# Optimization experiments

Measured on AMD Instinct MI355X. Metric: run time of the kernel, lower is better.

The kernel has to match this reference:

```python
import jax, jax.numpy as jnp
import numpy as np

N_NODES = 20000
N_EDGES = 200000
D_MODEL = 128
N_HEADS = 8
N_LAYERS = 2  # num_gnn - 1 concat layers


def setup_inputs() -> dict:
    key = jax.random.key(0)
    ks = jax.random.split(key, 12)
    s = 0.05  # keep activations well-scaled across residual layers
    hd = D_MODEL // N_HEADS  # 16
    return {
        "x": jax.random.normal(ks[0], (N_NODES, D_MODEL), jnp.float32),
        "src": jax.random.randint(ks[1], (N_EDGES,), 0, N_NODES),
        "dst": jax.random.randint(ks[2], (N_EDGES,), 0, N_NODES),
        "Ws": jax.random.normal(ks[3], (N_LAYERS, D_MODEL, D_MODEL), jnp.float32) * s,
        "als": jax.random.normal(ks[4], (N_LAYERS, N_HEADS, hd), jnp.float32) * s,
        "ars": jax.random.normal(ks[5], (N_LAYERS, N_HEADS, hd), jnp.float32) * s,
        "bs": jax.random.normal(ks[6], (N_LAYERS, D_MODEL), jnp.float32) * s,
        "W_last": jax.random.normal(ks[7], (D_MODEL, N_HEADS * D_MODEL), jnp.float32) * s,
        "al_last": jax.random.normal(ks[8], (N_HEADS, D_MODEL), jnp.float32) * s,
        "ar_last": jax.random.normal(ks[9], (N_HEADS, D_MODEL), jnp.float32) * s,
        "b_last": jax.random.normal(ks[10], (N_HEADS * D_MODEL,), jnp.float32) * s,
    }


def gat_conv(h, src, dst, W, al, ar, b, num_nodes):
    """DGL GATConv (eval mode, dropout off): returns (N, H, D) head outputs."""
    H, D = al.shape
    feat = (h @ W).reshape(num_nodes, H, D)          # (N,H,D)
    el = jnp.sum(feat * al[None], axis=-1)           # (N,H) attn on src side
    er = jnp.sum(feat * ar[None], axis=-1)           # (N,H) attn on dst side
    e = jax.nn.leaky_relu(el[src] + er[dst], 0.2)    # (E,H)
    # edge softmax over incoming edges of each dst node, per head
    m = jax.ops.segment_max(e, dst, num_segments=num_nodes)  # (N,H)
    p = jnp.exp(e - m[dst])                          # (E,H)
    z = jax.ops.segment_sum(p, dst, num_segments=num_nodes)  # (N,H)
    a = p / z[dst]                                   # (E,H)
    msg = feat[src] * a[..., None]                   # (E,H,D) weighted messages
    rst = jax.ops.segment_sum(msg, dst, num_segments=num_nodes)  # (N,H,D)
    return rst + b.reshape(1, H, D)


def reference(x, src, dst, Ws, als, ars, bs, W_last, al_last, ar_last, b_last):
    N = x.shape[0]
    h = x
    for i in range(N_LAYERS):
        temp = gat_conv(h, src, dst, Ws[i], als[i], ars[i], bs[i], N)  # (N,H,hd)
        h = h + jax.nn.elu(temp.reshape(N, -1))       # concat heads, ELU, residual
    temp = gat_conv(h, src, dst, W_last, al_last, ar_last, b_last, N)  # (N,H,D)
    h = h + jnp.mean(temp, axis=1)                    # mean over heads, residual
    return h
```

## Files before the change

kernel.cpp:

```cpp
#include <hip/hip_runtime.h>
#include <math.h>

#define N_NODES 20000
#define N_EDGES 200000
#define DM 128
#define NH 8

typedef __attribute__((ext_vector_type(8))) short bf16x8;
typedef __attribute__((ext_vector_type(4))) float f32x4;

__device__ __forceinline__ unsigned short f2b(float f) {
  unsigned int u = __float_as_uint(f);
  unsigned int r = (u + 0x7FFFu + ((u >> 16) & 1u)) >> 16;
  return (unsigned short)r;
}
__device__ __forceinline__ float b2f(unsigned short s) {
  return __uint_as_float(((unsigned int)s) << 16);
}

__global__ __launch_bounds__(256) void degzero(int* __restrict__ deg) {
  int i = blockIdx.x * 256 + threadIdx.x;
  if (i < N_NODES) deg[i] = 0;
}

__global__ __launch_bounds__(256) void prep_all(
    const float* __restrict__ x, float* __restrict__ h, unsigned short* __restrict__ hb,
    const int* __restrict__ dstE, int* __restrict__ deg, int* __restrict__ rank,
    const float* __restrict__ Ws, unsigned short* __restrict__ wsz,
    const float* __restrict__ W_last, unsigned short* __restrict__ wpsz,
    const float* __restrict__ al_last, const float* __restrict__ ar_last,
    const float* __restrict__ b_last, unsigned short* __restrict__ wlrsz,
    float* __restrict__ mb) {
  int i = blockIdx.x * 256 + threadIdx.x;
  if (i < (N_NODES * DM) / 4) {
    float4 v = ((const float4*)x)[i];
    ((float4*)h)[i] = v;
    ((ushort4*)hb)[i] = make_ushort4(f2b(v.x), f2b(v.y), f2b(v.z), f2b(v.w));
  }
  if (i < N_EDGES) rank[i] = atomicAdd(&deg[dstE[i]], 1);
  if (i < 2 * 16384) {
    int layer = i >> 14;
    int r = i & 16383;
    int j = r & 7, l = (r >> 3) & 63, f = (r >> 9) & 7, ks = r >> 12;
    int k = ks * 32 + ((l >> 4) << 3) + j;
    int n = f * 16 + (l & 15);
    wsz[i] = f2b(Ws[(size_t)layer * 16384 + k * 128 + n]);
  }
  if (i < 131072) {
    int j = i & 7, l = (i >> 3) & 63, f = (i >> 9) & 7, ks = i >> 12;
    int k = ks * 32 + ((l >> 4) << 3) + j;
    int n = f * 16 + (l & 15);
    int h_ = k >> 7, ko = k & 127;
    wpsz[i] = f2b(W_last[(size_t)ko * 1024 + h_ * 128 + n] * 0.125f);
  }
  if (i < 2048) {
    int j = i & 7, l = (i >> 3) & 63, ks = i >> 9;
    int k = ks * 32 + ((l >> 4) << 3) + j;
    int n = l & 15;
    int hh = n & 7;
    const float* av = (n < 8) ? (al_last + hh * 128) : (ar_last + hh * 128);
    float s = 0.f;
    for (int d = 0; d < 128; ++d) s += W_last[(size_t)k * 1024 + hh * 128 + d] * av[d];
    wlrsz[i] = f2b(s);
  }
  if (i < 128) {
    float s = 0.f;
#pragma unroll
    for (int hh = 0; hh < 8; ++hh) s += b_last[hh * 128 + i];
    mb[i] = s * 0.125f;
  }
}

__global__ void scan_deg(const int* __restrict__ deg, int* __restrict__ off) {
  __shared__ int part[1024];
  const int tid = threadIdx.x;
  const int CHUNK = (N_NODES + 1023) / 1024;
  int base = tid * CHUNK;
  int s = 0;
  for (int i = 0; i < CHUNK; ++i) {
    int idx = base + i;
    if (idx < N_NODES) s += deg[idx];
  }
  part[tid] = s;
  __syncthreads();
  for (int ofs = 1; ofs < 1024; ofs <<= 1) {
    int v = (tid >= ofs) ? part[tid - ofs] : 0;
    __syncthreads();
    part[tid] += v;
    __syncthreads();
  }
  int run = (tid > 0) ? part[tid - 1] : 0;
  for (int i = 0; i < CHUNK; ++i) {
    int idx = base + i;
    if (idx < N_NODES) {
      off[idx] = run;
      run += deg[idx];
    }
  }
  if (tid == 0) off[N_NODES] = part[1023];
}

template <int K>
__device__ __forceinline__ void dev_gemm(int tile, const unsigned short* __restrict__ A,
                                         const unsigned short* __restrict__ Bsz,
                                         unsigned short* __restrict__ Cb,
                                         const float* __restrict__ al,
                                         const float* __restrict__ ar,
                                         float* __restrict__ elr, int lane, int wid) {
  const int wrow = wid & 1, wc = wid >> 1;
  const int r0 = tile * 32;
  const int arow = r0 + wrow * 16 + (lane & 15);
  const int kg = lane >> 4;

  f32x4 acc[4];
#pragma unroll
  for (int fi = 0; fi < 4; ++fi) acc[fi] = {0.f, 0.f, 0.f, 0.f};

  const bf16x8* Ap = (const bf16x8*)(A + (size_t)arow * K + kg * 8);
#pragma unroll 4
  for (int ks = 0; ks < K / 32; ++ks) {
    bf16x8 a = Ap[ks * 4];
#pragma unroll
    for (int fi = 0; fi < 4; ++fi) {
      int f = wc * 4 + fi;
      bf16x8 b = *(const bf16x8*)(Bsz + (((size_t)(ks * 8 + f) * 64 + lane) << 3));
      acc[fi] = __builtin_amdgcn_mfma_f32_16x16x32_bf16(a, b, acc[fi], 0, 0, 0);
    }
  }

  const int rbase = r0 + wrow * 16 + (lane >> 4) * 4;
#pragma unroll
  for (int fi = 0; fi < 4; ++fi) {
    int col = wc * 64 + fi * 16 + (lane & 15);
#pragma unroll
    for (int r = 0; r < 4; ++r) {
      Cb[(size_t)(rbase + r) * DM + col] = f2b(acc[fi][r]);
    }
  }

#pragma unroll
  for (int fi = 0; fi < 4; ++fi) {
    int hh = wc * 4 + fi;
    float alv = al[hh * 16 + (lane & 15)];
    float arv = ar[hh * 16 + (lane & 15)];
#pragma unroll
    for (int r = 0; r < 4; ++r) {
      float pl = acc[fi][r] * alv;
      float pr = acc[fi][r] * arv;
#pragma unroll
      for (int msk = 1; msk < 16; msk <<= 1) {
        pl += __shfl_xor(pl, msk, 64);
        pr += __shfl_xor(pr, msk, 64);
      }
      if ((lane & 15) == 0) {
        int row = rbase + r;
        elr[row * 16 + hh] = pl;
        elr[row * 16 + 8 + hh] = pr;
      }
    }
  }
}

__global__ __launch_bounds__(256) void gemm0_scatter(
    const unsigned short* __restrict__ A, const unsigned short* __restrict__ Bsz,
    unsigned short* __restrict__ Cb, const float* __restrict__ al,
    const float* __restrict__ ar, float* __restrict__ elr, const int* __restrict__ srcE,
    const int* __restrict__ dstE, const int* __restrict__ rank,
    const int* __restrict__ off, int* __restrict__ csr_src) {
  const int bid = blockIdx.x;
  if (bid < N_NODES / 32) {
    dev_gemm<DM>(bid, A, Bsz, Cb, al, ar, elr, threadIdx.x & 63, threadIdx.x >> 6);
  } else {
    int e = (bid - N_NODES / 32) * 256 + threadIdx.x;
    if (e < N_EDGES) {
      csr_src[off[dstE[e]] + rank[e]] = srcE[e];
    }
  }
}

__global__ __launch_bounds__(256) void gemm_mfma(
    const unsigned short* __restrict__ A, const unsigned short* __restrict__ Bsz,
    unsigned short* __restrict__ Cb, const float* __restrict__ al,
    const float* __restrict__ ar, float* __restrict__ elr) {
  dev_gemm<DM>(blockIdx.x, A, Bsz, Cb, al, ar, elr, threadIdx.x & 63, threadIdx.x >> 6);
}

template <bool ELR>
__global__ __launch_bounds__(256) void fused_small(
    const int* __restrict__ off, const int* __restrict__ csr_src,
    const unsigned short* __restrict__ feat, const float* __restrict__ elr,
    const float* __restrict__ bias, float* __restrict__ h, unsigned short* __restrict__ hb,
    const unsigned short* __restrict__ wlrsz, float* __restrict__ elr_out) {
  __shared__ float a_lds[4][64];
  __shared__ int s_lds[4][8];
  __shared__ float zi_lds[4][8];
  __shared__ __align__(16) unsigned short nh_lds[4][128];
  const int wid = threadIdx.x >> 6;
  const int t = blockIdx.x * 4 + wid;
  const int lane = threadIdx.x & 63;
  const int e_loc = lane >> 3, hh = lane & 7;
  const int hg = lane >> 3;
  const int beg = off[t], end = off[t + 1];
  const float ert = elr[t * 16 + 8 + hh];

  int e = beg + e_loc;
  bool val = e < end;
  int s = val ? csr_src[e] : 0;
  float xl = val ? elr[s * 16 + hh] : 0.f;

  float z = 0.f, acc0 = 0.f, acc1 = 0.f;
  for (int base = beg; base < end; base += 8) {
    float ex = 0.f;
    if (val) {
      float xv = xl + ert;
      xv = xv > 0.f ? xv : 0.2f * xv;
      ex = __expf(xv);
    }
    a_lds[wid][lane] = ex;
    if (hh == 0) s_lds[wid][e_loc] = s;
    __builtin_amdgcn_wave_barrier();
    asm volatile("s_waitcnt lgkmcnt(0)" ::: "memory");
    z += ex;
    int en = base + 8 + e_loc;
    bool valn = en < end;
    int sn = valn ? csr_src[en] : 0;
    float xln = valn ? elr[sn * 16 + hh] : 0.f;
    int n = min(8, end - base);
    for (int e2 = 0; e2 < n; ++e2) {
      int s2 = s_lds[wid][e2];
      float a = a_lds[wid][e2 * 8 + hg];
      unsigned int hv = *(const unsigned int*)&feat[(size_t)s2 * 128 + 2 * lane];
      acc0 += a * b2f((unsigned short)(hv & 0xffffu));
      acc1 += a * b2f((unsigned short)(hv >> 16));
    }
    __builtin_amdgcn_wave_barrier();
    s = sn;
    xl = xln;
    val = valn;
  }
  z += __shfl_xor(z, 8, 64);
  z += __shfl_xor(z, 16, 64);
  z += __shfl_xor(z, 32, 64);
  if (e_loc == 0) zi_lds[wid][hh] = (z > 0.f) ? 1.f / z : 0.f;
  __builtin_amdgcn_wave_barrier();
  asm volatile("s_waitcnt lgkmcnt(0)" ::: "memory");
  float zi = zi_lds[wid][hg];

  float2 bv = *(const float2*)&bias[2 * lane];
  float v0 = acc0 * zi + bv.x;
  float v1 = acc1 * zi + bv.y;
  v0 = v0 > 0.f ? v0 : expm1f(v0);
  v1 = v1 > 0.f ? v1 : expm1f(v1);
  size_t idx = (size_t)t * 128 + 2 * lane;
  float2 hv = *(const float2*)&h[idx];
  float nh0 = hv.x + v0;
  float nh1 = hv.y + v1;
  *(float2*)&h[idx] = make_float2(nh0, nh1);
  unsigned short b0 = f2b(nh0), b1 = f2b(nh1);
  *(ushort2*)&hb[idx] = make_ushort2(b0, b1);

  if (ELR) {
    *(ushort2*)&nh_lds[wid][2 * lane] = make_ushort2(b0, b1);
    __builtin_amdgcn_wave_barrier();
    asm volatile("s_waitcnt lgkmcnt(0)" ::: "memory");
    const int kg = lane >> 4;
    f32x4 acc = {0.f, 0.f, 0.f, 0.f};
#pragma unroll
    for (int ks = 0; ks < 4; ++ks) {
      bf16x8 a = *(const bf16x8*)&nh_lds[wid][ks * 32 + kg * 8];
      bf16x8 b = *(const bf16x8*)(wlrsz + (((size_t)ks * 64 + lane) << 3));
      acc = __builtin_amdgcn_mfma_f32_16x16x32_bf16(a, b, acc, 0, 0, 0);
    }
    if (lane < 16) elr_out[t * 16 + lane] = acc[0];
  }
}

#define GT_STRIDE 1032
__global__ __launch_bounds__(1024) void agg_gemm16(
    const int* __restrict__ off, const int* __restrict__ csr_src,
    const unsigned short* __restrict__ hb, const float* __restrict__ elr,
    const unsigned short* __restrict__ wpsz, const float* __restrict__ hres,
    const float* __restrict__ mb, float* __restrict__ out) {
  __shared__ __align__(16) unsigned short gt[16][GT_STRIDE];
  __shared__ float red[8][64][4];
  __shared__ float a_lds[16][64];
  __shared__ int s_lds[16][8];
  __shared__ float zi_lds[16][8];
  const int wid = threadIdx.x >> 6;
  const int lane = threadIdx.x & 63;
  const int t0 = blockIdx.x * 16;
  const int t = t0 + wid;
  const int e_loc = lane >> 3, hh = lane & 7;

  {
    const int beg = off[t], end = off[t + 1];
    const float ert = elr[t * 16 + 8 + hh];
    int e = beg + e_loc;
    bool val = e < end;
    int s = val ? csr_src[e] : 0;
    float xl = val ? elr[s * 16 + hh] : 0.f;

    float z = 0.f;
    float accA[8], accB[8];
#pragma unroll
    for (int k = 0; k < 8; ++k) accA[k] = accB[k] = 0.f;

    for (int base = beg; base < end; base += 8) {
      float ex = 0.f;
      if (val) {
        float xv = xl + ert;
        xv = xv > 0.f ? xv : 0.2f * xv;
        ex = __expf(xv);
      }
      a_lds[wid][lane] = ex;
      if (hh == 0) s_lds[wid][e_loc] = s;
      __builtin_amdgcn_wave_barrier();
      asm volatile("s_waitcnt lgkmcnt(0)" ::: "memory");
      z += ex;
      int en = base + 8 + e_loc;
      bool valn = en < end;
      int sn = valn ? csr_src[en] : 0;
      float xln = valn ? elr[sn * 16 + hh] : 0.f;
      int n = min(8, end - base);
      for (int e2 = 0; e2 < n; ++e2) {
        int s2 = s_lds[wid][e2];
        float4 pa = *(const float4*)&a_lds[wid][e2 * 8];
        float4 pb = *(const float4*)&a_lds[wid][e2 * 8 + 4];
        unsigned int hv = *(const unsigned int*)&hb[(size_t)s2 * 128 + 2 * lane];
        float h0 = b2f((unsigned short)(hv & 0xffffu));
        float h1 = b2f((unsigned short)(hv >> 16));
        accA[0] += pa.x * h0; accB[0] += pa.x * h1;
        accA[1] += pa.y * h0; accB[1] += pa.y * h1;
        accA[2] += pa.z * h0; accB[2] += pa.z * h1;
        accA[3] += pa.w * h0; accB[3] += pa.w * h1;
        accA[4] += pb.x * h0; accB[4] += pb.x * h1;
        accA[5] += pb.y * h0; accB[5] += pb.y * h1;
        accA[6] += pb.z * h0; accB[6] += pb.z * h1;
        accA[7] += pb.w * h0; accB[7] += pb.w * h1;
      }
      __builtin_amdgcn_wave_barrier();
      s = sn;
      xl = xln;
      val = valn;
    }
    z += __shfl_xor(z, 8, 64);
    z += __shfl_xor(z, 16, 64);
    z += __shfl_xor(z, 32, 64);
    if (e_loc == 0) zi_lds[wid][hh] = (z > 0.f) ? 1.f / z : 0.f;
    __builtin_amdgcn_wave_barrier();
    asm volatile("s_waitcnt lgkmcnt(0)" ::: "memory");
    float4 zia = *(const float4*)&zi_lds[wid][0];
    float4 zib = *(const float4*)&zi_lds[wid][4];
    float ziv[8] = {zia.x, zia.y, zia.z, zia.w, zib.x, zib.y, zib.z, zib.w};
#pragma unroll
    for (int h2 = 0; h2 < 8; ++h2) {
      *(ushort2*)&gt[wid][h2 * 128 + 2 * lane] =
          make_ushort2(f2b(accA[h2] * ziv[h2]), f2b(accB[h2] * ziv[h2]));
    }
  }
  __syncthreads();

  const int f = wid & 7;
  const int kh = wid >> 3;
  const int ar16 = lane & 15;
  const int kg = lane >> 4;
  f32x4 acc = {0.f, 0.f, 0.f, 0.f};
#pragma unroll 4
  for (int ksl = 0; ksl < 16; ++ksl) {
    int ks = kh * 16 + ksl;
    bf16x8 a = *(const bf16x8*)&gt[ar16][ks * 32 + kg * 8];
    bf16x8 b = *(const bf16x8*)(wpsz + (((size_t)(ks * 8 + f) * 64 + lane) << 3));
    acc = __builtin_amdgcn_mfma_f32_16x16x32_bf16(a, b, acc, 0, 0, 0);
  }
  if (kh == 1) {
    *(float4*)&red[f][lane][0] = make_float4(acc[0], acc[1], acc[2], acc[3]);
  }
  __syncthreads();
  if (kh == 0) {
    float4 p = *(const float4*)&red[f][lane][0];
    const int col = f * 16 + (lane & 15);
    const int rb = (lane >> 4) * 4;
    float r4[4] = {p.x, p.y, p.z, p.w};
#pragma unroll
    for (int r = 0; r < 4; ++r) {
      int row = t0 + rb + r;
      out[(size_t)row * 128 + col] =
          acc[r] + r4[r] + hres[(size_t)row * 128 + col] + mb[col];
    }
  }
}

extern "C" void kernel_launch(void* const* d_in, const int* in_sizes, int n_in,
                              void* d_out, int out_size, void* d_ws, size_t ws_size,
                              hipStream_t stream) {
  const float* x = (const float*)d_in[0];
  const int* src = (const int*)d_in[1];
  const int* dst = (const int*)d_in[2];
  const float* Ws = (const float*)d_in[3];
  const float* als = (const float*)d_in[4];
  const float* ars = (const float*)d_in[5];
  const float* bs = (const float*)d_in[6];
  const float* W_last = (const float*)d_in[7];
  const float* al_last = (const float*)d_in[8];
  const float* ar_last = (const float*)d_in[9];
  const float* b_last = (const float*)d_in[10];
  float* out = (float*)d_out;

  float* h = (float*)d_ws;
  float* elr = h + 2560000;
  float* elr2 = elr + 320000;
  float* mb = elr2 + 320000;
  unsigned short* hb = (unsigned short*)(mb + 128);
  unsigned short* feat = hb + 2560000;
  unsigned short* wsz = feat + 2560000;
  unsigned short* wpsz = wsz + 32768;
  unsigned short* wlrsz = wpsz + 131072;
  int* deg = (int*)(wlrsz + 2048);
  int* off = deg + N_NODES;
  int* rank = off + N_NODES + 1;
  int* csr_src = rank + N_EDGES;

  const int GB = N_NODES / 32;
  const int FB = N_NODES / 4;
  const int EB = (N_EDGES + 255) / 256;

  degzero<<<(N_NODES + 255) / 256, 256, 0, stream>>>(deg);
  prep_all<<<(N_NODES * DM / 4 + 255) / 256, 256, 0, stream>>>(
      x, h, hb, dst, deg, rank, Ws, wsz, W_last, wpsz, al_last, ar_last, b_last, wlrsz, mb);
  scan_deg<<<1, 1024, 0, stream>>>(deg, off);
  gemm0_scatter<<<GB + EB, 256, 0, stream>>>(hb, wsz, feat, als, ars, elr, src, dst, rank,
                                             off, csr_src);
  fused_small<false><<<FB, 256, 0, stream>>>(off, csr_src, feat, elr, bs, h, hb, nullptr,
                                             nullptr);
  gemm_mfma<<<GB, 256, 0, stream>>>(hb, wsz + 16384, feat, als + 128, ars + 128, elr);
  fused_small<true><<<FB, 256, 0, stream>>>(off, csr_src, feat, elr, bs + 128, h, hb,
                                            wlrsz, elr2);
  agg_gemm16<<<N_NODES / 16, 1024, 0, stream>>>(off, csr_src, hb, elr2, wpsz, h, mb, out);
}
```

Baseline: 176.5 us.

## Fuse layer-1 GEMM into layer-0 aggregation epilogue and unroll full edge batches

Removes the separate gemm_mfma launch by computing the next layer's feature projection and attention logits inside fused_small's epilogue. Each block's four freshly updated node rows are fed through MFMA with the layer-1 weights, writing to new double-buffered feat/elr arrays to avoid read-write hazards. The inner edge loops also get a fully unrolled path for full 8-edge batches. The fused epilogue uses a 16-row MFMA with only 4 valid rows, wasting compute, and re-reads weights per block, in exchange for one fewer kernel launch and one fewer pass over hb.

```diff
diff --git a/kernel.cpp b/kernel.cpp
--- a/kernel.cpp
+++ b/kernel.cpp
@@ -178,19 +178,15 @@
   }
 }
 
-__global__ __launch_bounds__(256) void gemm_mfma(
-    const unsigned short* __restrict__ A, const unsigned short* __restrict__ Bsz,
-    unsigned short* __restrict__ Cb, const float* __restrict__ al,
-    const float* __restrict__ ar, float* __restrict__ elr) {
-  dev_gemm<DM>(blockIdx.x, A, Bsz, Cb, al, ar, elr, threadIdx.x & 63, threadIdx.x >> 6);
-}
-
-template <bool ELR>
+template <int MODE>
 __global__ __launch_bounds__(256) void fused_small(
     const int* __restrict__ off, const int* __restrict__ csr_src,
     const unsigned short* __restrict__ feat, const float* __restrict__ elr,
     const float* __restrict__ bias, float* __restrict__ h, unsigned short* __restrict__ hb,
-    const unsigned short* __restrict__ wlrsz, float* __restrict__ elr_out) {
+    const unsigned short* __restrict__ wsz1, const float* __restrict__ al1,
+    const float* __restrict__ ar1, unsigned short* __restrict__ feat_out,
+    float* __restrict__ elr_out, const unsigned short* __restrict__ wlrsz,
+    float* __restrict__ elr2_out) {
   __shared__ float a_lds[4][64];
   __shared__ int s_lds[4][8];
   __shared__ float zi_lds[4][8];
@@ -226,12 +222,23 @@
     int sn = valn ? csr_src[en] : 0;
     float xln = valn ? elr[sn * 16 + hh] : 0.f;
     int n = min(8, end - base);
-    for (int e2 = 0; e2 < n; ++e2) {
-      int s2 = s_lds[wid][e2];
-      float a = a_lds[wid][e2 * 8 + hg];
-      unsigned int hv = *(const unsigned int*)&feat[(size_t)s2 * 128 + 2 * lane];
-      acc0 += a * b2f((unsigned short)(hv & 0xffffu));
-      acc1 += a * b2f((unsigned short)(hv >> 16));
+    if (n == 8) {
+#pragma unroll
+      for (int e2 = 0; e2 < 8; ++e2) {
+        int s2 = s_lds[wid][e2];
+        float a = a_lds[wid][e2 * 8 + hg];
+        unsigned int hv = *(const unsigned int*)&feat[(size_t)s2 * 128 + 2 * lane];
+        acc0 += a * b2f((unsigned short)(hv & 0xffffu));
+        acc1 += a * b2f((unsigned short)(hv >> 16));
+      }
+    } else {
+      for (int e2 = 0; e2 < n; ++e2) {
+        int s2 = s_lds[wid][e2];
+        float a = a_lds[wid][e2 * 8 + hg];
+        unsigned int hv = *(const unsigned int*)&feat[(size_t)s2 * 128 + 2 * lane];
+        acc0 += a * b2f((unsigned short)(hv & 0xffffu));
+        acc1 += a * b2f((unsigned short)(hv >> 16));
+      }
     }
     __builtin_amdgcn_wave_barrier();
     s = sn;
@@ -258,9 +265,9 @@
   *(float2*)&h[idx] = make_float2(nh0, nh1);
   unsigned short b0 = f2b(nh0), b1 = f2b(nh1);
   *(ushort2*)&hb[idx] = make_ushort2(b0, b1);
-
-  if (ELR) {
-    *(ushort2*)&nh_lds[wid][2 * lane] = make_ushort2(b0, b1);
+  *(ushort2*)&nh_lds[wid][2 * lane] = make_ushort2(b0, b1);
+
+  if (MODE == 1) {
     __builtin_amdgcn_wave_barrier();
     asm volatile("s_waitcnt lgkmcnt(0)" ::: "memory");
     const int kg = lane >> 4;
@@ -271,7 +278,52 @@
       bf16x8 b = *(const bf16x8*)(wlrsz + (((size_t)ks * 64 + lane) << 3));
       acc = __builtin_amdgcn_mfma_f32_16x16x32_bf16(a, b, acc, 0, 0, 0);
     }
-    if (lane < 16) elr_out[t * 16 + lane] = acc[0];
+    if (lane < 16) elr2_out[t * 16 + lane] = acc[0];
+  }
+
+  if (MODE == 0) {
+    __syncthreads();
+    const int t0b = blockIdx.x * 4;
+    const int r16 = lane & 15;
+    const int kg = lane >> 4;
+    f32x4 acc2[2];
+    acc2[0] = {0.f, 0.f, 0.f, 0.f};
+    acc2[1] = {0.f, 0.f, 0.f, 0.f};
+#pragma unroll
+    for (int ks = 0; ks < 4; ++ks) {
+      bf16x8 a = {0, 0, 0, 0, 0, 0, 0, 0};
+      if (r16 < 4) a = *(const bf16x8*)&nh_lds[r16][ks * 32 + kg * 8];
+#pragma unroll
+      for (int fi = 0; fi < 2; ++fi) {
+        int f = wid * 2 + fi;
+        bf16x8 b = *(const bf16x8*)(wsz1 + (((size_t)(ks * 8 + f) * 64 + lane) << 3));
+        acc2[fi] = __builtin_amdgcn_mfma_f32_16x16x32_bf16(a, b, acc2[fi], 0, 0, 0);
+      }
+    }
+    const int rowl = (lane >> 4) * 4;
+#pragma unroll
+    for (int fi = 0; fi < 2; ++fi) {
+      int f = wid * 2 + fi;
+      int col = f * 16 + r16;
+      float alv = al1[col];
+      float arv = ar1[col];
+#pragma unroll
+      for (int r = 0; r < 4; ++r) {
+        float v = acc2[fi][r];
+        if (rowl == 0) feat_out[(size_t)(t0b + r) * 128 + col] = f2b(v);
+        float pl = v * alv;
+        float pr = v * arv;
+#pragma unroll
+        for (int msk = 1; msk < 16; msk <<= 1) {
+          pl += __shfl_xor(pl, msk, 64);
+          pr += __shfl_xor(pr, msk, 64);
+        }
+        if (r16 == 0 && rowl == 0) {
+          elr_out[(t0b + r) * 16 + f] = pl;
+          elr_out[(t0b + r) * 16 + 8 + f] = pr;
+        }
+      }
+    }
   }
 }
 
@@ -322,21 +374,41 @@
       int sn = valn ? csr_src[en] : 0;
       float xln = valn ? elr[sn * 16 + hh] : 0.f;
       int n = min(8, end - base);
-      for (int e2 = 0; e2 < n; ++e2) {
-        int s2 = s_lds[wid][e2];
-        float4 pa = *(const float4*)&a_lds[wid][e2 * 8];
-        float4 pb = *(const float4*)&a_lds[wid][e2 * 8 + 4];
-        unsigned int hv = *(const unsigned int*)&hb[(size_t)s2 * 128 + 2 * lane];
-        float h0 = b2f((unsigned short)(hv & 0xffffu));
-        float h1 = b2f((unsigned short)(hv >> 16));
-        accA[0] += pa.x * h0; accB[0] += pa.x * h1;
-        accA[1] += pa.y * h0; accB[1] += pa.y * h1;
-        accA[2] += pa.z * h0; accB[2] += pa.z * h1;
-        accA[3] += pa.w * h0; accB[3] += pa.w * h1;
-        accA[4] += pb.x * h0; accB[4] += pb.x * h1;
-        accA[5] += pb.y * h0; accB[5] += pb.y * h1;
-        accA[6] += pb.z * h0; accB[6] += pb.z * h1;
-        accA[7] += pb.w * h0; accB[7] += pb.w * h1;
+      if (n == 8) {
+#pragma unroll
+        for (int e2 = 0; e2 < 8; ++e2) {
+          int s2 = s_lds[wid][e2];
+          float4 pa = *(const float4*)&a_lds[wid][e2 * 8];
+          float4 pb = *(const float4*)&a_lds[wid][e2 * 8 + 4];
+          unsigned int hv = *(const unsigned int*)&hb[(size_t)s2 * 128 + 2 * lane];
+          float h0 = b2f((unsigned short)(hv & 0xffffu));
+          float h1 = b2f((unsigned short)(hv >> 16));
+          accA[0] += pa.x * h0; accB[0] += pa.x * h1;
+          accA[1] += pa.y * h0; accB[1] += pa.y * h1;
+          accA[2] += pa.z * h0; accB[2] += pa.z * h1;
+          accA[3] += pa.w * h0; accB[3] += pa.w * h1;
+          accA[4] += pb.x * h0; accB[4] += pb.x * h1;
+          accA[5] += pb.y * h0; accB[5] += pb.y * h1;
+          accA[6] += pb.z * h0; accB[6] += pb.z * h1;
+          accA[7] += pb.w * h0; accB[7] += pb.w * h1;
+        }
+      } else {
+        for (int e2 = 0; e2 < n; ++e2) {
+          int s2 = s_lds[wid][e2];
+          float4 pa = *(const float4*)&a_lds[wid][e2 * 8];
+          float4 pb = *(const float4*)&a_lds[wid][e2 * 8 + 4];
+          unsigned int hv = *(const unsigned int*)&hb[(size_t)s2 * 128 + 2 * lane];
+          float h0 = b2f((unsigned short)(hv & 0xffffu));
+          float h1 = b2f((unsigned short)(hv >> 16));
+          accA[0] += pa.x * h0; accB[0] += pa.x * h1;
+          accA[1] += pa.y * h0; accB[1] += pa.y * h1;
+          accA[2] += pa.z * h0; accB[2] += pa.z * h1;
+          accA[3] += pa.w * h0; accB[3] += pa.w * h1;
+          accA[4] += pb.x * h0; accB[4] += pb.x * h1;
+          accA[5] += pb.y * h0; accB[5] += pb.y * h1;
+          accA[6] += pb.z * h0; accB[6] += pb.z * h1;
+          accA[7] += pb.w * h0; accB[7] += pb.w * h1;
+        }
       }
       __builtin_amdgcn_wave_barrier();
       s = sn;
@@ -407,12 +479,14 @@
   float* out = (float*)d_out;
 
   float* h = (float*)d_ws;
-  float* elr = h + 2560000;
-  float* elr2 = elr + 320000;
+  float* elr0 = h + 2560000;
+  float* elrB = elr0 + 320000;
+  float* elr2 = elrB + 320000;
   float* mb = elr2 + 320000;
   unsigned short* hb = (unsigned short*)(mb + 128);
-  unsigned short* feat = hb + 2560000;
-  unsigned short* wsz = feat + 2560000;
+  unsigned short* featA = hb + 2560000;
+  unsigned short* featB = featA + 2560000;
+  unsigned short* wsz = featB + 2560000;
   unsigned short* wpsz = wsz + 32768;
   unsigned short* wlrsz = wpsz + 131072;
   int* deg = (int*)(wlrsz + 2048);
@@ -428,12 +502,13 @@
   prep_all<<<(N_NODES * DM / 4 + 255) / 256, 256, 0, stream>>>(
       x, h, hb, dst, deg, rank, Ws, wsz, W_last, wpsz, al_last, ar_last, b_last, wlrsz, mb);
   scan_deg<<<1, 1024, 0, stream>>>(deg, off);
-  gemm0_scatter<<<GB + EB, 256, 0, stream>>>(hb, wsz, feat, als, ars, elr, src, dst, rank,
-                                             off, csr_src);
-  fused_small<false><<<FB, 256, 0, stream>>>(off, csr_src, feat, elr, bs, h, hb, nullptr,
-                                             nullptr);
-  gemm_mfma<<<GB, 256, 0, stream>>>(hb, wsz + 16384, feat, als + 128, ars + 128, elr);
-  fused_small<true><<<FB, 256, 0, stream>>>(off, csr_src, feat, elr, bs + 128, h, hb,
-                                            wlrsz, elr2);
+  gemm0_scatter<<<GB + EB, 256, 0, stream>>>(hb, wsz, featA, als, ars, elr0, src, dst,
+                                             rank, off, csr_src);
+  fused_small<0><<<FB, 256, 0, stream>>>(off, csr_src, featA, elr0, bs, h, hb,
+                                         wsz + 16384, als + 128, ars + 128, featB, elrB,
+                                         nullptr, nullptr);
+  fused_small<1><<<FB, 256, 0, stream>>>(off, csr_src, featB, elrB, bs + 128, h, hb,
+                                         nullptr, nullptr, nullptr, nullptr, nullptr,
+                                         wlrsz, elr2);
   agg_gemm16<<<N_NODES / 16, 1024, 0, stream>>>(off, csr_src, hb, elr2, wpsz, h, mb, out);
 }
```

Result: faster. 167.6 us (-5.0%).
